# Performance work log

Hardware: AMD Instinct MI355X
Metric: run time of the kernel (lower is better)

The kernel has to match this reference:

```python
import jax, jax.numpy as jnp
import numpy as np

B, S, F, D, H, L, K = 64, 512, 8, 512, 8, 2, 512
FF = 4 * D
DH = D // H


def _ln(x):
    m = jnp.mean(x, axis=-1, keepdims=True)
    v = jnp.var(x, axis=-1, keepdims=True)
    return (x - m) * jax.lax.rsqrt(v + 1e-5)


def _encoder_layer(x, Wqkv, Wo, W1, b1, W2, b2):
    # pre-LN multi-head self-attention
    h = _ln(x)
    qkv = h @ Wqkv                                   # [B,S,3D]
    q, k, v = jnp.split(qkv, 3, axis=-1)
    q = q.reshape(B, S, H, DH)
    k = k.reshape(B, S, H, DH)
    v = v.reshape(B, S, H, DH)
    scores = jnp.einsum('bqhd,bkhd->bhqk', q, k) / jnp.sqrt(jnp.float32(DH))
    attn = jax.nn.softmax(scores, axis=-1)
    o = jnp.einsum('bhqk,bkhd->bqhd', attn, v).reshape(B, S, D) @ Wo
    x = x + o
    # pre-LN feed-forward
    h = _ln(x)
    x = x + (jax.nn.relu(h @ W1 + b1) @ W2 + b2)
    return x


def setup_inputs() -> dict:
    key = jax.random.key(0)
    ks = jax.random.split(key, 12)
    sc = 0.02
    inp = {
        'x': jax.random.normal(ks[0], (B, S, F), dtype=jnp.float32),
        'enc_W': jax.random.normal(ks[1], (F, D), dtype=jnp.float32) * sc,
        'enc_b': jnp.zeros((D,), dtype=jnp.float32),
        'Wqkv': jax.random.normal(ks[2], (L, D, 3 * D), dtype=jnp.float32) * sc,
        'Wo': jax.random.normal(ks[3], (L, D, D), dtype=jnp.float32) * sc,
        'W1': jax.random.normal(ks[4], (L, D, FF), dtype=jnp.float32) * sc,
        'b1': jnp.zeros((L, FF), dtype=jnp.float32),
        'W2': jax.random.normal(ks[5], (L, FF, D), dtype=jnp.float32) * sc,
        'b2': jnp.zeros((L, D), dtype=jnp.float32),
        'centers': jax.random.normal(ks[6], (K, D), dtype=jnp.float32),
    }
    return inp


def reference(x, enc_W, enc_b, Wqkv, Wo, W1, b1, W2, b2, centers):
    # enc_embedding
    h = x @ enc_W + enc_b                            # [B,S,D]
    # seq_model: stack of standard transformer encoder layers
    for i in range(L):
        h = _encoder_layer(h, Wqkv[i], Wo[i], W1[i], b1[i], W2[i], b2[i])
    output_seq = h                                   # [B,S,D]
    # torch.cdist(output_seq, centers, p=2) via matmul expansion
    on2 = jnp.sum(output_seq * output_seq, axis=-1, keepdims=True)   # [B,S,1]
    cn2 = jnp.sum(centers * centers, axis=-1)                        # [K]
    dist2 = on2 + cn2[None, None, :] - 2.0 * jnp.einsum('bsd,kd->bsk', output_seq, centers)
    cluster_ids = jnp.argmin(dist2, axis=-1)                         # [B,S]
    assigned_centroids = centers[cluster_ids]                        # [B,S,D] gather
    diff = output_seq - assigned_centroids
    # torch.norm(diff, dim=1)**2 then mean == mean over (B,D) of sum over S of diff^2
    loss = jnp.mean(jnp.sum(diff * diff, axis=1))
    return loss, output_seq
```

## Files before the change

### kernel.cpp

```cpp
#include <hip/hip_runtime.h>
#include <cstdint>
#include <cstddef>

typedef __attribute__((ext_vector_type(4))) float f32x4;
typedef __attribute__((ext_vector_type(8))) short s16x8;
typedef __attribute__((ext_vector_type(4))) short s16x4;

__device__ __forceinline__ short f2bf(float f){
  unsigned u; __builtin_memcpy(&u, &f, 4);
  u += 0x7fffu + ((u >> 16) & 1u);
  return (short)(u >> 16);
}

__device__ __forceinline__ void gll16(const void* g, void* l) {
  auto* lp = (__attribute__((address_space(3))) unsigned*)(uintptr_t)(l);
  const auto* gp = (const __attribute__((address_space(1))) unsigned*)(uintptr_t)(g);
  __builtin_amdgcn_global_load_lds(gp, lp, 16, 0, 0);
}

__device__ __forceinline__ void ds_tr8(unsigned a, s16x4* r) {
  asm volatile(
    "ds_read_b64_tr_b16 %0, %8\n\t"
    "ds_read_b64_tr_b16 %1, %8 offset:512\n\t"
    "ds_read_b64_tr_b16 %2, %8 offset:2048\n\t"
    "ds_read_b64_tr_b16 %3, %8 offset:2560\n\t"
    "ds_read_b64_tr_b16 %4, %8 offset:4096\n\t"
    "ds_read_b64_tr_b16 %5, %8 offset:4608\n\t"
    "ds_read_b64_tr_b16 %6, %8 offset:6144\n\t"
    "ds_read_b64_tr_b16 %7, %8 offset:6656\n\t"
    "s_waitcnt lgkmcnt(0)"
    : "=&v"(r[0]), "=&v"(r[1]), "=&v"(r[2]), "=&v"(r[3]),
      "=&v"(r[4]), "=&v"(r[5]), "=&v"(r[6]), "=&v"(r[7])
    : "v"(a)
    : "memory");
}

__device__ __forceinline__ int pidx(int m, int k, int ntk) {
  return ((m >> 4) * ntk + (k >> 5)) * 512 + ((((k >> 3) & 3) * 16 + (m & 15)) << 3) + (k & 7);
}

__global__ __launch_bounds__(256) void encode_kernel(
    const float* __restrict__ x, const float* __restrict__ W,
    const float* __restrict__ b, float* __restrict__ out)
{
  const int t = blockIdx.x;
  float xv[8];
#pragma unroll
  for (int f = 0; f < 8; ++f) xv[f] = x[(size_t)t*8 + f];
  for (int d = threadIdx.x; d < 512; d += 256) {
    float acc = b[d];
#pragma unroll
    for (int f = 0; f < 8; ++f) acc += xv[f] * W[f*512 + d];
    out[(size_t)t*512 + d] = acc;
  }
}

__global__ __launch_bounds__(256) void ln_kernel(
    const float* __restrict__ x, short* __restrict__ out)
{
  const int w = threadIdx.x >> 6, lane = threadIdx.x & 63;
  const int t = blockIdx.x * 4 + w;
  const float* row = x + (size_t)t * 512;
  float4 v0 = *(const float4*)&row[lane*8];
  float4 v1 = *(const float4*)&row[lane*8 + 4];
  float vals[8] = {v0.x,v0.y,v0.z,v0.w,v1.x,v1.y,v1.z,v1.w};
  float s = 0.f, sq = 0.f;
#pragma unroll
  for (int i = 0; i < 8; ++i) { s += vals[i]; sq += vals[i]*vals[i]; }
#pragma unroll
  for (int m = 1; m < 64; m <<= 1) { s += __shfl_xor(s, m); sq += __shfl_xor(sq, m); }
  float mean = s * (1.f/512.f);
  float var  = sq * (1.f/512.f) - mean*mean;
  float rstd = rsqrtf(var + 1e-5f);
  s16x8 o;
#pragma unroll
  for (int i = 0; i < 8; ++i) o[i] = f2bf((vals[i]-mean)*rstd);
  *(s16x8*)&out[pidx(t, lane*8, 16)] = o;
}

__global__ __launch_bounds__(256) void packB_kernel(
    const float* __restrict__ in, short* __restrict__ out, int K, int N)
{
  const int n = blockIdx.x * 256 + threadIdx.x;
  const int k = blockIdx.y;
  out[pidx(n, k, K >> 5)] = f2bf(in[(size_t)k * N + n]);
}

__global__ __launch_bounds__(256) void packBNK_kernel(
    const float* __restrict__ in, short* __restrict__ out, int K, int N)
{
  const int k = blockIdx.x * 256 + threadIdx.x;
  const int n = blockIdx.y;
  out[pidx(n, k, K >> 5)] = f2bf(in[(size_t)n * K + k]);
}

template<bool BIAS, bool RELU, bool RESID, int OUTMODE>
__global__ __launch_bounds__(512, 1) void gemm_kernel(
    const short* __restrict__ Ap, const short* __restrict__ Bp,
    void* Cout, const float* __restrict__ bias,
    const float* resid, short* __restrict__ obf, int M, int N, int K)
{
  __shared__ short As[4][16 * 512];
  const int tid = threadIdx.x;
  const int lane = tid & 63, w = tid >> 6;
  const int wr = w >> 2, wc = w & 3;
  const int q = lane & 15, g = lane >> 4;

  const int nx = gridDim.x;
  const int d = blockIdx.y * nx + blockIdx.x;
  const int per = (nx * gridDim.y) >> 3;
  const int lid = (d & 7) * per + (d >> 3);
  const int bx = lid % nx, by = lid / nx;
  const int m0 = by * 256, n0 = bx * 256;

  const int nt = K >> 5;
  const size_t pstride = (size_t)nt * 512;

  const short* aP = Ap + ((size_t)(m0 >> 4) + w) * pstride + lane * 8;
  const short* bp0 = Bp + ((size_t)(n0 >> 4) + wc * 4) * pstride + lane * 8;

  f32x4 acc[8][4] = {};

  auto STAGE_A = [&](int tt) {
    const int nb = tt & 3;
    gll16(aP + (size_t)tt * 512,               &As[nb][w * 512]);
    gll16(aP + 8 * pstride + (size_t)tt * 512, &As[nb][(8 + w) * 512]);
  };
  s16x8 bA[4], bB[4];
  auto LOADB = [&](int tt, s16x8* bf) {
#pragma unroll
    for (int i = 0; i < 4; ++i)
      bf[i] = *(const s16x8*)&bp0[(size_t)i * pstride + (size_t)tt * 512];
  };
  auto TILE = [&](int t, s16x8* bcur, s16x8* bnxt, bool doLB, bool doSA) {
    __builtin_amdgcn_s_barrier();
    __builtin_amdgcn_sched_barrier(0);
    if (doLB) LOADB(t + 1, bnxt);
    __builtin_amdgcn_sched_barrier(0);
    if (doSA) STAGE_A(t + 3);
    __builtin_amdgcn_sched_barrier(0);
    const short* Ab = &As[t & 3][0];
    s16x8 aF[8];
#pragma unroll
    for (int i = 0; i < 8; ++i) aF[i] = *(const s16x8*)&Ab[(wr*8 + i)*512 + lane*8];
    __builtin_amdgcn_s_setprio(1);
#pragma unroll
    for (int mi = 0; mi < 8; ++mi)
#pragma unroll
      for (int ni = 0; ni < 4; ++ni)
        acc[mi][ni] = __builtin_amdgcn_mfma_f32_16x16x32_bf16(aF[mi], bcur[ni], acc[mi][ni], 0, 0, 0);
    __builtin_amdgcn_s_setprio(0);
  };

  STAGE_A(0);
  LOADB(0, bA);
  STAGE_A(1);
  STAGE_A(2);

  for (int t = 0; t < nt - 2; t += 2) {
    asm volatile("s_waitcnt vmcnt(8)" ::: "memory");
    TILE(t, bA, bB, true, true);
    asm volatile("s_waitcnt vmcnt(8)" ::: "memory");
    TILE(t + 1, bB, bA, true, t + 4 < nt);
  }
  asm volatile("s_waitcnt vmcnt(6)" ::: "memory");
  TILE(nt - 2, bA, bB, true, false);
  asm volatile("s_waitcnt vmcnt(4)" ::: "memory");
  TILE(nt - 1, bB, bA, false, false);

  const int ntk_out = N >> 5;
#pragma unroll
  for (int mi = 0; mi < 8; ++mi) {
#pragma unroll
    for (int r = 0; r < 4; ++r) {
      const int gr = m0 + wr*128 + mi*16 + g*4 + r;
#pragma unroll
      for (int ni = 0; ni < 4; ++ni) {
        const int gc = n0 + wc*64 + ni*16 + q;
        float v = acc[mi][ni][r];
        if (BIAS) v += bias[gc];
        if (RELU) v = fmaxf(v, 0.f);
        if (RESID) v += resid[(size_t)gr * N + gc];
        if (OUTMODE == 0)      ((short*)Cout)[(size_t)gr * N + gc] = f2bf(v);
        else if (OUTMODE == 1) ((short*)Cout)[pidx(gr, gc, ntk_out)] = f2bf(v);
        else if (OUTMODE == 2) ((float*)Cout)[(size_t)gr * N + gc] = v;
        else { ((float*)Cout)[(size_t)gr * N + gc] = v; obf[pidx(gr, gc, ntk_out)] = f2bf(v); }
      }
    }
  }
}

__global__ __launch_bounds__(256) void attn_kernel(
    const short* __restrict__ qkv, short* __restrict__ attn_out)
{
  __shared__ short Ks[2][64 * 64];
  __shared__ short Vs[2][64 * 64];
  const int tid = threadIdx.x;
  const int w = tid >> 6, lane = tid & 63;
  const int q16 = lane & 15, g = lane >> 4;
  const int dd = blockIdx.x;
  const int lid = (dd & 7) * (int)(gridDim.x >> 3) + (dd >> 3);
  const int qt4 = lid & 7, h = (lid >> 3) & 7, b = lid >> 6;
  const size_t base = (size_t)b * 512 * 1536;
  const int qrow = qt4*64 + w*16 + q16;

  s16x8 bQ0, bQ1;
  {
    const size_t p = base + (size_t)qrow * 1536 + h*64 + g*8;
    bQ0 = *(const s16x8*)&qkv[p];
    bQ1 = *(const s16x8*)&qkv[p + 32];
  }

  const int c0 = w*2, c1 = w*2 + 1;
  const short* kS0 = qkv + base + (size_t)(c0*8 + (lane>>3))*1536 + 512 + h*64 + ((lane&7)^(lane>>3))*8;
  const short* kS1 = qkv + base + (size_t)(c1*8 + (lane>>3))*1536 + 512 + h*64 + ((lane&7)^(lane>>3))*8;
  const short* vS0 = qkv + base + (size_t)((c0&1)*32 + (lane>>1))*1536 + 1024 + h*64 + (c0>>1)*16 + (lane&1)*8;
  const short* vS1 = qkv + base + (size_t)((c1&1)*32 + (lane>>1))*1536 + 1024 + h*64 + (c1>>1)*16 + (lane&1)*8;

  const unsigned vs_lane = (unsigned)(size_t)(&Vs[0][0]) + (unsigned)((q16 + g*64)*2);
  const int sw = q16 & 7;

  float mrun = -1e30f, ssum = 0.f;
  f32x4 O[4] = {};

  gll16(kS0, &Ks[0][c0*512]);
  gll16(kS1, &Ks[0][c1*512]);
  gll16(vS0, &Vs[0][c0*512]);
  gll16(vS1, &Vs[0][c1*512]);
  __syncthreads();

  int cur = 0;
  for (int j0 = 0; j0 < 512; j0 += 64) {
    s16x8 ka0[4], ka1[4];
#pragma unroll
    for (int grp = 0; grp < 4; ++grp) {
      const int rb = (grp*16 + q16) * 64;
      ka0[grp] = *(const s16x8*)&Ks[cur][rb + ((g    ) ^ sw)*8];
      ka1[grp] = *(const s16x8*)&Ks[cur][rb + ((g + 4) ^ sw)*8];
    }
    if (j0 + 64 < 512) {
      const size_t joff = (size_t)(j0 + 64) * 1536;
      const int nxt = cur ^ 1;
      gll16(kS0 + joff, &Ks[nxt][c0*512]);
      gll16(kS1 + joff, &Ks[nxt][c1*512]);
      gll16(vS0 + joff, &Vs[nxt][c0*512]);
      gll16(vS1 + joff, &Vs[nxt][c1*512]);
    }
    __builtin_amdgcn_sched_barrier(0);

    f32x4 c[4];
    __builtin_amdgcn_s_setprio(1);
#pragma unroll
    for (int grp = 0; grp < 4; ++grp) {
      f32x4 z = {};
      c[grp] = __builtin_amdgcn_mfma_f32_16x16x32_bf16(ka0[grp], bQ0, z, 0, 0, 0);
      c[grp] = __builtin_amdgcn_mfma_f32_16x16x32_bf16(ka1[grp], bQ1, c[grp], 0, 0, 0);
    }
    __builtin_amdgcn_s_setprio(0);

    float sc[16];
#pragma unroll
    for (int grp = 0; grp < 4; ++grp)
#pragma unroll
      for (int r = 0; r < 4; ++r) sc[grp*4 + r] = c[grp][r] * 0.125f;
    float bm = sc[0];
#pragma unroll
    for (int i = 1; i < 16; ++i) bm = fmaxf(bm, sc[i]);
    bm = fmaxf(bm, __shfl_xor(bm, 16));
    bm = fmaxf(bm, __shfl_xor(bm, 32));
    const float mn = fmaxf(mrun, bm);
    const float alpha = __expf(mrun - mn);
    float p[16]; float bs = 0.f;
#pragma unroll
    for (int i = 0; i < 16; ++i) { p[i] = __expf(sc[i] - mn); bs += p[i]; }
    bs += __shfl_xor(bs, 16);
    bs += __shfl_xor(bs, 32);
    ssum = ssum * alpha + bs;
    mrun = mn;
#pragma unroll
    for (int db = 0; db < 4; ++db) O[db] *= alpha;

#pragma unroll
    for (int kk = 0; kk < 2; ++kk) {
      s16x8 pf;
#pragma unroll
      for (int e = 0; e < 8; ++e) pf[e] = f2bf(p[(kk*2 + (e >> 2))*4 + (e & 3)]);
      s16x4 r[8];
      ds_tr8(vs_lane + (unsigned)(cur << 13) + (unsigned)(kk*1024), r);
      __builtin_amdgcn_sched_barrier(0);
      __builtin_amdgcn_s_setprio(1);
#pragma unroll
      for (int db = 0; db < 4; ++db) {
        s16x8 vf = __builtin_shufflevector(r[2*db], r[2*db + 1], 0, 1, 2, 3, 4, 5, 6, 7);
        O[db] = __builtin_amdgcn_mfma_f32_16x16x32_bf16(vf, pf, O[db], 0, 0, 0);
      }
      __builtin_amdgcn_s_setprio(0);
    }
    __syncthreads();
    cur ^= 1;
  }

  const float inv = 1.f / ssum;
  const int tok = b*512 + qrow;
#pragma unroll
  for (int db = 0; db < 4; ++db) {
    s16x4 ov;
#pragma unroll
    for (int r = 0; r < 4; ++r) ov[r] = f2bf(O[db][r] * inv);
    const int d0 = h*64 + db*16 + g*4;
    *(s16x4*)&attn_out[pidx(tok, d0, 16)] = ov;
  }
}

__global__ __launch_bounds__(256) void cn2_kernel(
    const float* __restrict__ centers, float* __restrict__ cn2)
{
  const int c = blockIdx.x;
  __shared__ float red[256];
  float s = 0.f;
  for (int d = threadIdx.x; d < 512; d += 256) { float v = centers[(size_t)c*512 + d]; s += v*v; }
  red[threadIdx.x] = s; __syncthreads();
  for (int off = 128; off > 0; off >>= 1) {
    if (threadIdx.x < off) red[threadIdx.x] += red[threadIdx.x + off];
    __syncthreads();
  }
  if (threadIdx.x == 0) cn2[c] = red[0];
}

__global__ __launch_bounds__(256) void argmin_kernel(
    const float* __restrict__ gdist, const float* __restrict__ cn2,
    const float* __restrict__ seq, const float* __restrict__ centers,
    float* __restrict__ partial)
{
  const int w = threadIdx.x >> 6, lane = threadIdx.x & 63;
  const int t = blockIdx.x * 4 + w;
  float best = 1e30f; int bi = 0;
#pragma unroll
  for (int j = 0; j < 8; ++j) {
    const int k = j*64 + lane;
    const float v = cn2[k] - 2.f * gdist[(size_t)t*512 + k];
    if (v < best || (v == best && k < bi)) { best = v; bi = k; }
  }
#pragma unroll
  for (int mm = 1; mm < 64; mm <<= 1) {
    const float ov = __shfl_xor(best, mm); const int oi = __shfl_xor(bi, mm);
    if (ov < best || (ov == best && oi < bi)) { best = ov; bi = oi; }
  }
  float s = 0.f;
#pragma unroll
  for (int j = 0; j < 8; ++j) {
    const int dcol = j*64 + lane;
    const float o = seq[(size_t)t*512 + dcol];
    const float c = centers[(size_t)bi*512 + dcol];
    const float dv = o - c;
    s += dv * dv;
  }
#pragma unroll
  for (int mm = 1; mm < 64; mm <<= 1) s += __shfl_xor(s, mm);
  __shared__ float red[4];
  if (lane == 0) red[w] = s;
  __syncthreads();
  if (threadIdx.x == 0) partial[blockIdx.x] = red[0] + red[1] + red[2] + red[3];
}

__global__ __launch_bounds__(256) void loss_kernel(
    const float* __restrict__ partial, int n, float* __restrict__ out)
{
  float s = 0.f;
  for (int i = threadIdx.x; i < n; i += 256) s += partial[i];
  __shared__ float red[256];
  red[threadIdx.x] = s; __syncthreads();
  for (int off = 128; off > 0; off >>= 1) {
    if (threadIdx.x < off) red[threadIdx.x] += red[threadIdx.x + off];
    __syncthreads();
  }
  if (threadIdx.x == 0) out[0] = red[0] * (1.f / 32768.f);
}

extern "C" void kernel_launch(void* const* d_in, const int* in_sizes, int n_in,
                              void* d_out, int out_size, void* d_ws, size_t ws_size,
                              hipStream_t stream) {
  const float* x     = (const float*)d_in[0];
  const float* enc_W = (const float*)d_in[1];
  const float* enc_b = (const float*)d_in[2];
  const float* Wqkv  = (const float*)d_in[3];
  const float* Wo    = (const float*)d_in[4];
  const float* W1    = (const float*)d_in[5];
  const float* b1    = (const float*)d_in[6];
  const float* W2    = (const float*)d_in[7];
  const float* b2    = (const float*)d_in[8];
  const float* cen   = (const float*)d_in[9];
  float* out = (float*)d_out;

  const int NT = 32768;
  char* ws = (char*)d_ws;
  float* resid   = (float*)(ws);
  short* h_ln    = (short*)(ws + 67108864);
  char*  pool    = ws + 100663296;
  short* qkv     = (short*)pool;
  short* attn_o  = (short*)(pool + 100663296);
  short* hidden  = (short*)pool;
  float* gdist   = (float*)pool;
  short* wbase   = (short*)(ws + 234881024);
  short* wqP     = wbase;
  short* woP     = wbase + 1572864;
  short* w1P     = wbase + 2097152;
  short* w2P     = wbase + 4194304;
  short* cenb    = wbase + 6291456;
  float* cn2     = (float*)(ws + 247988224);
  float* partial = (float*)(ws + 247990272);

  for (int l = 0; l < 2; ++l) {
    packB_kernel<<<dim3(6, 512), 256, 0, stream>>>(Wqkv + (size_t)l*512*1536, wqP + (size_t)l*786432, 512, 1536);
    packB_kernel<<<dim3(2, 512), 256, 0, stream>>>(Wo   + (size_t)l*512*512,  woP + (size_t)l*262144, 512, 512);
    packB_kernel<<<dim3(8, 512), 256, 0, stream>>>(W1   + (size_t)l*512*2048, w1P + (size_t)l*1048576, 512, 2048);
    packB_kernel<<<dim3(2, 2048), 256, 0, stream>>>(W2  + (size_t)l*2048*512, w2P + (size_t)l*1048576, 2048, 512);
  }
  packBNK_kernel<<<dim3(2, 512), 256, 0, stream>>>(cen, cenb, 512, 512);
  cn2_kernel<<<512, 256, 0, stream>>>(cen, cn2);

  encode_kernel<<<NT, 256, 0, stream>>>(x, enc_W, enc_b, resid);

  for (int l = 0; l < 2; ++l) {
    ln_kernel<<<NT/4, 256, 0, stream>>>(resid, h_ln);
    gemm_kernel<false,false,false,0><<<dim3(6, 128), 512, 0, stream>>>(
        h_ln, wqP + (size_t)l*786432, qkv, nullptr, nullptr, nullptr, NT, 1536, 512);
    attn_kernel<<<4096, 256, 0, stream>>>(qkv, attn_o);
    gemm_kernel<false,false,true,2><<<dim3(2, 128), 512, 0, stream>>>(
        attn_o, woP + (size_t)l*262144, resid, nullptr, resid, nullptr, NT, 512, 512);
    ln_kernel<<<NT/4, 256, 0, stream>>>(resid, h_ln);
    gemm_kernel<true,true,false,1><<<dim3(8, 128), 512, 0, stream>>>(
        h_ln, w1P + (size_t)l*1048576, hidden, b1 + (size_t)l*2048, nullptr, nullptr, NT, 2048, 512);
    if (l == 0) {
      gemm_kernel<true,false,true,2><<<dim3(2, 128), 512, 0, stream>>>(
          hidden, w2P + (size_t)l*1048576, resid, b2 + (size_t)l*512, resid, nullptr, NT, 512, 2048);
    } else {
      gemm_kernel<true,false,true,3><<<dim3(2, 128), 512, 0, stream>>>(
          hidden, w2P + (size_t)l*1048576, out + 1, b2 + (size_t)l*512, resid, h_ln, NT, 512, 2048);
    }
  }

  gemm_kernel<false,false,false,2><<<dim3(2, 128), 512, 0, stream>>>(
      h_ln, cenb, gdist, nullptr, nullptr, nullptr, NT, 512, 512);
  argmin_kernel<<<NT/4, 256, 0, stream>>>(gdist, cn2, out + 1, cen, partial);
  loss_kernel<<<1, 256, 0, stream>>>(partial, NT/4, out);
}
```

Baseline: 934.6 us.

## Store residual stream in bf16 and use 128-row GEMM tiles for N=512 GEMMs

The residual stream is now kept in bf16 rather than fp32, which halves its read and write traffic in encode, layernorm and the residual-add GEMM epilogues. A new gemm128 kernel with 128x256 tiles and launch_bounds allowing several blocks per CU replaces the 256x256 kernel for the N=512 GEMMs (Wo, W2, centroid distances), giving a 512-block grid instead of 256 so the CUs are filled better. The cost is extra rounding error, since the residual accumulates in bf16 across layers, which could move argmin cluster assignments and the loss away from the fp32 reference.

```diff
diff --git a/kernel.cpp b/kernel.cpp
--- a/kernel.cpp
+++ b/kernel.cpp
@@ -10,6 +10,11 @@
   unsigned u; __builtin_memcpy(&u, &f, 4);
   u += 0x7fffu + ((u >> 16) & 1u);
   return (short)(u >> 16);
+}
+__device__ __forceinline__ float bf2f(short s){
+  unsigned u = ((unsigned)(unsigned short)s) << 16;
+  float f; __builtin_memcpy(&f, &u, 4);
+  return f;
 }
 
 __device__ __forceinline__ void gll16(const void* g, void* l) {
@@ -41,7 +46,7 @@
 
 __global__ __launch_bounds__(256) void encode_kernel(
     const float* __restrict__ x, const float* __restrict__ W,
-    const float* __restrict__ b, float* __restrict__ out)
+    const float* __restrict__ b, short* __restrict__ out)
 {
   const int t = blockIdx.x;
   float xv[8];
@@ -51,19 +56,19 @@
     float acc = b[d];
 #pragma unroll
     for (int f = 0; f < 8; ++f) acc += xv[f] * W[f*512 + d];
-    out[(size_t)t*512 + d] = acc;
+    out[(size_t)t*512 + d] = f2bf(acc);
   }
 }
 
 __global__ __launch_bounds__(256) void ln_kernel(
-    const float* __restrict__ x, short* __restrict__ out)
+    const short* __restrict__ x16, short* __restrict__ out)
 {
   const int w = threadIdx.x >> 6, lane = threadIdx.x & 63;
   const int t = blockIdx.x * 4 + w;
-  const float* row = x + (size_t)t * 512;
-  float4 v0 = *(const float4*)&row[lane*8];
-  float4 v1 = *(const float4*)&row[lane*8 + 4];
-  float vals[8] = {v0.x,v0.y,v0.z,v0.w,v1.x,v1.y,v1.z,v1.w};
+  s16x8 v = *(const s16x8*)&x16[(size_t)t*512 + lane*8];
+  float vals[8];
+#pragma unroll
+  for (int i = 0; i < 8; ++i) vals[i] = bf2f(v[i]);
   float s = 0.f, sq = 0.f;
 #pragma unroll
   for (int i = 0; i < 8; ++i) { s += vals[i]; sq += vals[i]*vals[i]; }
@@ -94,11 +99,10 @@
   out[pidx(n, k, K >> 5)] = f2bf(in[(size_t)n * K + k]);
 }
 
-template<bool BIAS, bool RELU, bool RESID, int OUTMODE>
-__global__ __launch_bounds__(512, 1) void gemm_kernel(
+template<bool BIAS, bool RELU, int OUTMODE>
+__global__ __launch_bounds__(512, 1) void gemm256_kernel(
     const short* __restrict__ Ap, const short* __restrict__ Bp,
-    void* Cout, const float* __restrict__ bias,
-    const float* resid, short* __restrict__ obf, int M, int N, int K)
+    void* Cout, const float* __restrict__ bias, int M, int N, int K)
 {
   __shared__ short As[4][16 * 512];
   const int tid = threadIdx.x;
@@ -115,8 +119,7 @@
 
   const int nt = K >> 5;
   const size_t pstride = (size_t)nt * 512;
-
-  const short* aP = Ap + ((size_t)(m0 >> 4) + w) * pstride + lane * 8;
+  const short* aP  = Ap + ((size_t)(m0 >> 4) + w) * pstride + lane * 8;
   const short* bp0 = Bp + ((size_t)(n0 >> 4) + wc * 4) * pstride + lane * 8;
 
   f32x4 acc[8][4] = {};
@@ -152,10 +155,7 @@
     __builtin_amdgcn_s_setprio(0);
   };
 
-  STAGE_A(0);
-  LOADB(0, bA);
-  STAGE_A(1);
-  STAGE_A(2);
+  STAGE_A(0); LOADB(0, bA); STAGE_A(1); STAGE_A(2);
 
   for (int t = 0; t < nt - 2; t += 2) {
     asm volatile("s_waitcnt vmcnt(8)" ::: "memory");
@@ -180,11 +180,97 @@
         float v = acc[mi][ni][r];
         if (BIAS) v += bias[gc];
         if (RELU) v = fmaxf(v, 0.f);
-        if (RESID) v += resid[(size_t)gr * N + gc];
-        if (OUTMODE == 0)      ((short*)Cout)[(size_t)gr * N + gc] = f2bf(v);
-        else if (OUTMODE == 1) ((short*)Cout)[pidx(gr, gc, ntk_out)] = f2bf(v);
-        else if (OUTMODE == 2) ((float*)Cout)[(size_t)gr * N + gc] = v;
-        else { ((float*)Cout)[(size_t)gr * N + gc] = v; obf[pidx(gr, gc, ntk_out)] = f2bf(v); }
+        if (OUTMODE == 0) ((short*)Cout)[(size_t)gr * N + gc] = f2bf(v);
+        else              ((short*)Cout)[pidx(gr, gc, ntk_out)] = f2bf(v);
+      }
+    }
+  }
+}
+
+template<bool BIAS, bool RESID16, int OUTMODE>
+__global__ __launch_bounds__(512, 4) void gemm128_kernel(
+    const short* __restrict__ Ap, const short* __restrict__ Bp,
+    void* Cout, const float* __restrict__ bias,
+    const short* __restrict__ resid16, short* __restrict__ obf, int M, int N, int K)
+{
+  __shared__ short As[4][8 * 512];
+  const int tid = threadIdx.x;
+  const int lane = tid & 63, w = tid >> 6;
+  const int wr = w >> 2, wc = w & 3;
+  const int q = lane & 15, g = lane >> 4;
+
+  const int nx = gridDim.x;
+  const int d = blockIdx.y * nx + blockIdx.x;
+  const int per = (nx * gridDim.y) >> 3;
+  const int lid = (d & 7) * per + (d >> 3);
+  const int bx = lid % nx, by = lid / nx;
+  const int m0 = by * 128, n0 = bx * 256;
+
+  const int nt = K >> 5;
+  const size_t pstride = (size_t)nt * 512;
+  const short* aP  = Ap + ((size_t)(m0 >> 4) + w) * pstride + lane * 8;
+  const short* bp0 = Bp + ((size_t)(n0 >> 4) + wc * 4) * pstride + lane * 8;
+
+  f32x4 acc[4][4] = {};
+
+  auto STAGE_A = [&](int tt) {
+    gll16(aP + (size_t)tt * 512, &As[tt & 3][w * 512]);
+  };
+  s16x8 bA[4], bB[4];
+  auto LOADB = [&](int tt, s16x8* bf) {
+#pragma unroll
+    for (int i = 0; i < 4; ++i)
+      bf[i] = *(const s16x8*)&bp0[(size_t)i * pstride + (size_t)tt * 512];
+  };
+  auto TILE = [&](int t, s16x8* bcur, s16x8* bnxt, bool doLB, bool doSA) {
+    __builtin_amdgcn_s_barrier();
+    __builtin_amdgcn_sched_barrier(0);
+    if (doLB) LOADB(t + 1, bnxt);
+    __builtin_amdgcn_sched_barrier(0);
+    if (doSA) STAGE_A(t + 3);
+    __builtin_amdgcn_sched_barrier(0);
+    const short* Ab = &As[t & 3][0];
+    s16x8 aF[4];
+#pragma unroll
+    for (int i = 0; i < 4; ++i) aF[i] = *(const s16x8*)&Ab[(wr*4 + i)*512 + lane*8];
+    __builtin_amdgcn_s_setprio(1);
+#pragma unroll
+    for (int mi = 0; mi < 4; ++mi)
+#pragma unroll
+      for (int ni = 0; ni < 4; ++ni)
+        acc[mi][ni] = __builtin_amdgcn_mfma_f32_16x16x32_bf16(aF[mi], bcur[ni], acc[mi][ni], 0, 0, 0);
+    __builtin_amdgcn_s_setprio(0);
+  };
+
+  STAGE_A(0); LOADB(0, bA); STAGE_A(1); STAGE_A(2);
+
+  for (int t = 0; t < nt - 2; t += 2) {
+    asm volatile("s_waitcnt vmcnt(6)" ::: "memory");
+    TILE(t, bA, bB, true, true);
+    asm volatile("s_waitcnt vmcnt(6)" ::: "memory");
+    TILE(t + 1, bB, bA, true, t + 4 < nt);
+  }
+  asm volatile("s_waitcnt vmcnt(5)" ::: "memory");
+  TILE(nt - 2, bA, bB, true, false);
+  asm volatile("s_waitcnt vmcnt(4)" ::: "memory");
+  TILE(nt - 1, bB, bA, false, false);
+
+  const int ntk_out = N >> 5;
+#pragma unroll
+  for (int mi = 0; mi < 4; ++mi) {
+#pragma unroll
+    for (int r = 0; r < 4; ++r) {
+      const int gr = m0 + wr*64 + mi*16 + g*4 + r;
+#pragma unroll
+      for (int ni = 0; ni < 4; ++ni) {
+        const int gc = n0 + wc*64 + ni*16 + q;
+        float v = acc[mi][ni][r];
+        if (BIAS) v += bias[gc];
+        if (RESID16) v += bf2f(resid16[(size_t)gr * N + gc]);
+        const size_t idx = (size_t)gr * N + gc;
+        if (OUTMODE == 0)      ((short*)Cout)[idx] = f2bf(v);
+        else if (OUTMODE == 2) ((float*)Cout)[idx] = v;
+        else { ((float*)Cout)[idx] = v; obf[pidx(gr, gc, ntk_out)] = f2bf(v); }
       }
     }
   }
@@ -394,7 +480,7 @@
 
   const int NT = 32768;
   char* ws = (char*)d_ws;
-  float* resid   = (float*)(ws);
+  short* resid16 = (short*)(ws);
   short* h_ln    = (short*)(ws + 67108864);
   char*  pool    = ws + 100663296;
   short* qkv     = (short*)pool;
@@ -419,28 +505,28 @@
   packBNK_kernel<<<dim3(2, 512), 256, 0, stream>>>(cen, cenb, 512, 512);
   cn2_kernel<<<512, 256, 0, stream>>>(cen, cn2);
 
-  encode_kernel<<<NT, 256, 0, stream>>>(x, enc_W, enc_b, resid);
+  encode_kernel<<<NT, 256, 0, stream>>>(x, enc_W, enc_b, resid16);
 
   for (int l = 0; l < 2; ++l) {
-    ln_kernel<<<NT/4, 256, 0, stream>>>(resid, h_ln);
-    gemm_kernel<false,false,false,0><<<dim3(6, 128), 512, 0, stream>>>(
-        h_ln, wqP + (size_t)l*786432, qkv, nullptr, nullptr, nullptr, NT, 1536, 512);
+    ln_kernel<<<NT/4, 256, 0, stream>>>(resid16, h_ln);
+    gemm256_kernel<false,false,0><<<dim3(6, 128), 512, 0, stream>>>(
+        h_ln, wqP + (size_t)l*786432, qkv, nullptr, NT, 1536, 512);
     attn_kernel<<<4096, 256, 0, stream>>>(qkv, attn_o);
-    gemm_kernel<false,false,true,2><<<dim3(2, 128), 512, 0, stream>>>(
-        attn_o, woP + (size_t)l*262144, resid, nullptr, resid, nullptr, NT, 512, 512);
-    ln_kernel<<<NT/4, 256, 0, stream>>>(resid, h_ln);
-    gemm_kernel<true,true,false,1><<<dim3(8, 128), 512, 0, stream>>>(
-        h_ln, w1P + (size_t)l*1048576, hidden, b1 + (size_t)l*2048, nullptr, nullptr, NT, 2048, 512);
+    gemm128_kernel<false,true,0><<<dim3(2, 256), 512, 0, stream>>>(
+        attn_o, woP + (size_t)l*262144, resid16, nullptr, resid16, nullptr, NT, 512, 512);
+    ln_kernel<<<NT/4, 256, 0, stream>>>(resid16, h_ln);
+    gemm256_kernel<true,true,1><<<dim3(8, 128), 512, 0, stream>>>(
+        h_ln, w1P + (size_t)l*1048576, hidden, b1 + (size_t)l*2048, NT, 2048, 512);
     if (l == 0) {
-      gemm_kernel<true,false,true,2><<<dim3(2, 128), 512, 0, stream>>>(
-          hidden, w2P + (size_t)l*1048576, resid, b2 + (size_t)l*512, resid, nullptr, NT, 512, 2048);
+      gemm128_kernel<true,true,0><<<dim3(2, 256), 512, 0, stream>>>(
+          hidden, w2P + (size_t)l*1048576, resid16, b2 + (size_t)l*512, resid16, nullptr, NT, 512, 2048);
     } else {
-      gemm_kernel<true,false,true,3><<<dim3(2, 128), 512, 0, stream>>>(
-          hidden, w2P + (size_t)l*1048576, out + 1, b2 + (size_t)l*512, resid, h_ln, NT, 512, 2048);
-    }
-  }
-
-  gemm_kernel<false,false,false,2><<<dim3(2, 128), 512, 0, stream>>>(
+      gemm128_kernel<true,true,3><<<dim3(2, 256), 512, 0, stream>>>(
+          hidden, w2P + (size_t)l*1048576, out + 1, b2 + (size_t)l*512, resid16, h_ln, NT, 512, 2048);
+    }
+  }
+
+  gemm128_kernel<false,false,2><<<dim3(2, 256), 512, 0, stream>>>(
       h_ln, cenb, gdist, nullptr, nullptr, nullptr, NT, 512, 512);
   argmin_kernel<<<NT/4, 256, 0, stream>>>(gdist, cn2, out + 1, cen, partial);
   loss_kernel<<<1, 256, 0, stream>>>(partial, NT/4, out);
```

Result: slower. 1.237 ms (+32.4%).
